# Kernel optimization log

Hardware: AMD Instinct MI355X
Metric: run time of the kernel (lower is better)

## Reference

```python
import jax, jax.numpy as jnp
import numpy as np

DIM = 1024
DIM_QK = 1024
DIM_V = 1024
H = 16
SCALE = 1.0 / (DIM_QK ** 0.5)  # NOTE: module scales by sqrt(dim_qk), not sqrt(head_dim)


def setup_inputs() -> dict:
    key = jax.random.key(0)
    ks = jax.random.split(key, 12)
    B, S = 2, 2048
    q = jax.random.normal(ks[0], (B, S, DIM), jnp.float32)
    k = jax.random.normal(ks[1], (B, S, DIM), jnp.float32)
    v = jax.random.normal(ks[2], (B, S, DIM), jnp.float32)
    mask = jax.random.randint(ks[3], (B, 1, S, S), 0, 2) > 0  # True = masked
    s = 1.0 / np.sqrt(DIM)
    Wq = jax.random.uniform(ks[4], (DIM_QK, DIM), jnp.float32, -s, s)
    bq = jax.random.uniform(ks[5], (DIM_QK,), jnp.float32, -s, s)
    Wk = jax.random.uniform(ks[6], (DIM_QK, DIM), jnp.float32, -s, s)
    bk = jax.random.uniform(ks[7], (DIM_QK,), jnp.float32, -s, s)
    Wv = jax.random.uniform(ks[8], (DIM_V, DIM), jnp.float32, -s, s)
    bv = jax.random.uniform(ks[9], (DIM_V,), jnp.float32, -s, s)
    Wo = jax.random.uniform(ks[10], (DIM_V, DIM), jnp.float32, -s, s)
    bo = jax.random.uniform(ks[11], (DIM_V,), jnp.float32, -s, s)
    return {"q": q, "k": k, "v": v, "mask": mask,
            "Wq": Wq, "bq": bq, "Wk": Wk, "bk": bk,
            "Wv": Wv, "bv": bv, "Wo": Wo, "bo": bo}


def reference(q, k, v, mask, Wq, bq, Wk, bk, Wv, bv, Wo, bo):
    B, Sq, _ = q.shape
    Skv = k.shape[1]
    # projections (torch Linear: x @ W.T + b)
    qh = (q @ Wq.T + bq).reshape(B, Sq, H, DIM_QK // H).transpose(0, 2, 1, 3)   # [B,H,Sq,dk]
    kh = (k @ Wk.T + bk).reshape(B, Skv, H, DIM_QK // H).transpose(0, 2, 1, 3)  # [B,H,Skv,dk]
    vh = (v @ Wv.T + bv).reshape(B, Skv, H, DIM_V // H).transpose(0, 2, 1, 3)   # [B,H,Skv,dv]
    attn = jnp.einsum('bhqd,bhkd->bhqk', qh, kh) * SCALE
    attn = jnp.where(mask, jnp.float32(-1e20), attn)
    attn = jax.nn.softmax(attn, axis=-1)
    # dropout is identity in eval / p=0
    out = jnp.einsum('bhqk,bhkd->bhqd', attn, vh)            # [B,H,Sq,dv]
    out = out.transpose(0, 2, 1, 3).reshape(B, Sq, DIM_V)
    return out @ Wo.T + bo
```

## Files before the change

kernel.cpp:

```cpp
#include <hip/hip_runtime.h>
#include <hip/hip_bf16.h>

typedef __attribute__((ext_vector_type(8))) __bf16 bf16x8;
typedef __attribute__((ext_vector_type(4))) short short4v;
typedef __attribute__((ext_vector_type(4))) float f32x4;
typedef __attribute__((ext_vector_type(4))) unsigned int uint4v;
typedef __attribute__((ext_vector_type(2))) unsigned int uint2v;

#define S_LEN 2048
#define DIM_  1024
#define HDIM  64
#define SCALE2 0.045084441f
#define QK_STR 80
#define V_STR  72

#define EXP2F(x) __builtin_amdgcn_exp2f(x)

__device__ __forceinline__ void async_copy16(const void* gp, void* lp) {
  __builtin_amdgcn_global_load_lds(
      (const __attribute__((address_space(1))) unsigned int*)gp,
      (__attribute__((address_space(3))) unsigned int*)lp, 16, 0, 0);
}

__device__ __forceinline__ unsigned f2bf_u(float f) {
  unsigned u = __builtin_bit_cast(unsigned, f);
  return (u + 0x7FFFu + ((u >> 16) & 1u)) >> 16;
}
__device__ __forceinline__ unsigned pack2(float a, float b) {
  return f2bf_u(a) | (f2bf_u(b) << 16);
}
__device__ __forceinline__ unsigned pack2f(float a, float b) {
  unsigned ua = __builtin_bit_cast(unsigned, a) + 0x8000u;
  unsigned ub = __builtin_bit_cast(unsigned, b) + 0x8000u;
  return __builtin_amdgcn_perm(ub, ua, 0x07060302u);
}

__global__ __launch_bounds__(256) void cvt_kernel(
    const float* __restrict__ s0, const float* __restrict__ s1, const float* __restrict__ s2,
    const float* __restrict__ s3, const float* __restrict__ s4, const float* __restrict__ s5,
    const float* __restrict__ s6,
    __hip_bfloat16* __restrict__ d0, __hip_bfloat16* __restrict__ d1, __hip_bfloat16* __restrict__ d2,
    __hip_bfloat16* __restrict__ d3, __hip_bfloat16* __restrict__ d4, __hip_bfloat16* __restrict__ d5,
    __hip_bfloat16* __restrict__ d6)
{
  const float* srcs[7] = {s0, s1, s2, s3, s4, s5, s6};
  __hip_bfloat16* dsts[7] = {d0, d1, d2, d3, d4, d5, d6};
  const int sizes[7] = {4194304, 4194304, 4194304, 1048576, 1048576, 1048576, 1048576};
  int rg = blockIdx.y;
  int base = (blockIdx.x * 256 + threadIdx.x) * 8;
  if (base >= sizes[rg]) return;
  const float* s = srcs[rg] + base;
  f32x4 a = *(const f32x4*)s;
  f32x4 b = *(const f32x4*)(s + 4);
  uint4v o;
  o.x = pack2(a[0], a[1]); o.y = pack2(a[2], a[3]);
  o.z = pack2(b[0], b[1]); o.w = pack2(b[2], b[3]);
  *(uint4v*)(dsts[rg] + base) = o;
}

__global__ __launch_bounds__(256) void maskbits_kernel(
    const int* __restrict__ mask, unsigned long long* __restrict__ bits)
{
  int w = (blockIdx.x * 256 + threadIdx.x) >> 6;
  int lane = threadIdx.x & 63;
  int m = mask[(size_t)w * 64 + lane];
  unsigned long long bal = __ballot(m != 0);
  if (lane == 0) bits[w] = bal;
}

__device__ __forceinline__ void swz(int r, int& m0, int& n0) {
  int g  = r >> 6;
  int yy = (r >> 3) & 7;
  int xl = r & 7;
  m0 = (g * 8 + xl) * 128;
  n0 = yy * 128;
}

__global__ __launch_bounds__(256) void qkv_gemm_kernel(
    const __hip_bfloat16* __restrict__ xq, const __hip_bfloat16* __restrict__ xk,
    const __hip_bfloat16* __restrict__ xv,
    const __hip_bfloat16* __restrict__ Wq, const float* __restrict__ bq,
    const __hip_bfloat16* __restrict__ Wk, const float* __restrict__ bk,
    const __hip_bfloat16* __restrict__ Wv, const float* __restrict__ bv,
    __hip_bfloat16* __restrict__ Q, __hip_bfloat16* __restrict__ Kk,
    __hip_bfloat16* __restrict__ VT)
{
  const __hip_bfloat16 *X, *W; const float* bias;
  if (blockIdx.z == 0)      { X = xq; W = Wq; bias = bq; }
  else if (blockIdx.z == 1) { X = xk; W = Wk; bias = bk; }
  else                      { X = xv; W = Wv; bias = bv; }

  constexpr int K = 1024, N = 1024;
  __shared__ alignas(16) __hip_bfloat16 As[2][128 * 32];
  __shared__ alignas(16) __hip_bfloat16 Bs[2][128 * 32];
  const int tid  = threadIdx.x;
  const int lane = tid & 63;
  const int wave = tid >> 6;
  const int t    = lane & 15;
  const int quad = lane >> 4;
  const int wm   = wave >> 1;
  const int wn   = wave & 1;
  int m0, n0;
  swz(blockIdx.x, m0, n0);

  f32x4 acc[4][4] = {};

  const int c0 = tid, c1 = 256 + tid;
  const int r0 = c0 >> 2, o0 = (c0 & 3) * 8;
  const int r1 = c1 >> 2, o1 = (c1 & 3) * 8;
  const __hip_bfloat16* xp0 = &X[(size_t)(m0 + r0) * K + o0];
  const __hip_bfloat16* xp1 = &X[(size_t)(m0 + r1) * K + o1];
  const __hip_bfloat16* wp0 = &W[(size_t)(n0 + r0) * K + o0];
  const __hip_bfloat16* wp1 = &W[(size_t)(n0 + r1) * K + o1];

  async_copy16(xp0, &As[0][c0 * 8]);
  async_copy16(xp1, &As[0][c1 * 8]);
  async_copy16(wp0, &Bs[0][c0 * 8]);
  async_copy16(wp1, &Bs[0][c1 * 8]);

  int buf = 0;
  for (int k0 = 0; k0 < K; k0 += 32) {
    __syncthreads();
    if (k0 + 32 < K) {
      int nb = buf ^ 1;
      int kn = k0 + 32;
      async_copy16(xp0 + kn, &As[nb][c0 * 8]);
      async_copy16(xp1 + kn, &As[nb][c1 * 8]);
      async_copy16(wp0 + kn, &Bs[nb][c0 * 8]);
      async_copy16(wp1 + kn, &Bs[nb][c1 * 8]);
    }
    bf16x8 a[4], b[4];
#pragma unroll
    for (int i = 0; i < 4; ++i)
      a[i] = *(const bf16x8*)&As[buf][(wm * 64 + i * 16 + t) * 32 + quad * 8];
#pragma unroll
    for (int j = 0; j < 4; ++j)
      b[j] = *(const bf16x8*)&Bs[buf][(wn * 64 + j * 16 + t) * 32 + quad * 8];
#pragma unroll
    for (int i = 0; i < 4; ++i)
#pragma unroll
      for (int j = 0; j < 4; ++j)
        acc[i][j] = __builtin_amdgcn_mfma_f32_16x16x32_bf16(a[i], b[j], acc[i][j], 0, 0, 0);
    buf ^= 1;
  }

  float bj[4];
#pragma unroll
  for (int j = 0; j < 4; ++j)
    bj[j] = bias[n0 + wn * 64 + j * 16 + t];

  if (blockIdx.z == 2) {
#pragma unroll
    for (int i = 0; i < 4; ++i)
#pragma unroll
      for (int j = 0; j < 4; ++j) {
        int m = m0 + wm * 64 + i * 16 + quad * 4;
        int n = n0 + wn * 64 + j * 16 + t;
        int bb = m >> 11, kv = m & 2047;
        int hh = n >> 6,  dv = n & 63;
        uint2v o;
        o.x = pack2(acc[i][j][0] + bj[j], acc[i][j][1] + bj[j]);
        o.y = pack2(acc[i][j][2] + bj[j], acc[i][j][3] + bj[j]);
        *(uint2v*)&VT[(size_t)(((bb * 16 + hh) * 64) + dv) * 2048 + kv] = o;
      }
  } else {
    const bool isq = (blockIdx.z == 0);
    __hip_bfloat16* Out = isq ? Q : Kk;
    const float sc = isq ? SCALE2 : 1.0f;
#pragma unroll
    for (int i = 0; i < 4; ++i)
#pragma unroll
      for (int j = 0; j < 4; ++j)
#pragma unroll
        for (int r = 0; r < 4; ++r) {
          int m = m0 + wm * 64 + i * 16 + quad * 4 + r;
          int n = n0 + wn * 64 + j * 16 + t;
          Out[(size_t)m * N + n] = __float2bfloat16((acc[i][j][r] + bj[j]) * sc);
        }
  }
}

__global__ __launch_bounds__(256) void proj_gemm_kernel(
    const __hip_bfloat16* __restrict__ X, const __hip_bfloat16* __restrict__ W,
    const float* __restrict__ bias, float* __restrict__ Out)
{
  constexpr int K = 1024, N = 1024;
  __shared__ alignas(16) __hip_bfloat16 As[2][128 * 32];
  __shared__ alignas(16) __hip_bfloat16 Bs[2][128 * 32];
  const int tid  = threadIdx.x;
  const int lane = tid & 63;
  const int wave = tid >> 6;
  const int t    = lane & 15;
  const int quad = lane >> 4;
  const int wm   = wave >> 1;
  const int wn   = wave & 1;
  int m0, n0;
  swz(blockIdx.x, m0, n0);

  f32x4 acc[4][4] = {};

  const int c0 = tid, c1 = 256 + tid;
  const int r0 = c0 >> 2, o0 = (c0 & 3) * 8;
  const int r1 = c1 >> 2, o1 = (c1 & 3) * 8;
  const __hip_bfloat16* xp0 = &X[(size_t)(m0 + r0) * K + o0];
  const __hip_bfloat16* xp1 = &X[(size_t)(m0 + r1) * K + o1];
  const __hip_bfloat16* wp0 = &W[(size_t)(n0 + r0) * K + o0];
  const __hip_bfloat16* wp1 = &W[(size_t)(n0 + r1) * K + o1];

  async_copy16(xp0, &As[0][c0 * 8]);
  async_copy16(xp1, &As[0][c1 * 8]);
  async_copy16(wp0, &Bs[0][c0 * 8]);
  async_copy16(wp1, &Bs[0][c1 * 8]);

  int buf = 0;
  for (int k0 = 0; k0 < K; k0 += 32) {
    __syncthreads();
    if (k0 + 32 < K) {
      int nb = buf ^ 1;
      int kn = k0 + 32;
      async_copy16(xp0 + kn, &As[nb][c0 * 8]);
      async_copy16(xp1 + kn, &As[nb][c1 * 8]);
      async_copy16(wp0 + kn, &Bs[nb][c0 * 8]);
      async_copy16(wp1 + kn, &Bs[nb][c1 * 8]);
    }
    bf16x8 a[4], b[4];
#pragma unroll
    for (int i = 0; i < 4; ++i)
      a[i] = *(const bf16x8*)&As[buf][(wm * 64 + i * 16 + t) * 32 + quad * 8];
#pragma unroll
    for (int j = 0; j < 4; ++j)
      b[j] = *(const bf16x8*)&Bs[buf][(wn * 64 + j * 16 + t) * 32 + quad * 8];
#pragma unroll
    for (int i = 0; i < 4; ++i)
#pragma unroll
      for (int j = 0; j < 4; ++j)
        acc[i][j] = __builtin_amdgcn_mfma_f32_16x16x32_bf16(a[i], b[j], acc[i][j], 0, 0, 0);
    buf ^= 1;
  }

  float bj[4];
#pragma unroll
  for (int j = 0; j < 4; ++j)
    bj[j] = bias[n0 + wn * 64 + j * 16 + t];
#pragma unroll
  for (int i = 0; i < 4; ++i)
#pragma unroll
    for (int j = 0; j < 4; ++j)
#pragma unroll
      for (int r = 0; r < 4; ++r) {
        int m = m0 + wm * 64 + i * 16 + quad * 4 + r;
        int n = n0 + wn * 64 + j * 16 + t;
        Out[(size_t)m * N + n] = acc[i][j][r] + bj[j];
      }
}

__global__ __launch_bounds__(256) void attn_kernel(
    const __hip_bfloat16* __restrict__ Qb,
    const __hip_bfloat16* __restrict__ Kb,
    const __hip_bfloat16* __restrict__ VT,
    const unsigned long long* __restrict__ mbits,
    __hip_bfloat16* __restrict__ Ob)
{
  const int bid = blockIdx.x;
  const int qt = bid & 31;
  const int h  = (bid >> 5) & 15;
  const int b  = bid >> 9;
  const int qb = qt * 64;

  __shared__ alignas(16) __hip_bfloat16 Qs[64 * QK_STR];
  __shared__ alignas(16) __hip_bfloat16 Ks[64 * QK_STR];
  __shared__ alignas(16) __hip_bfloat16 Vt[64 * V_STR];

  const int tid  = threadIdx.x;
  const int lane = tid & 63;
  const int wave = tid >> 6;
  const int t    = lane & 15;
  const int quad = lane >> 4;

#pragma unroll
  for (int r = 0; r < 2; ++r) {
    int c = r * 256 + tid;
    int row = c >> 3, d0 = (c & 7) * 8;
    uint4 raw = *(const uint4*)&Qb[((size_t)(b * S_LEN + qb + row)) * DIM_ + h * HDIM + d0];
    *(uint4*)&Qs[row * QK_STR + d0] = raw;
  }
  __syncthreads();

  bf16x8 qf[2];
#pragma unroll
  for (int ks = 0; ks < 2; ++ks)
    qf[ks] = *(const bf16x8*)&Qs[(wave * 16 + t) * QK_STR + ks * 32 + quad * 8];

  float lp = 0.f;
  f32x4 o[4] = {};

  const int qg = qb + wave * 16 + t;
  const size_t vtbase = (size_t)((b * 16 + h) * 64) * 2048;
  const size_t mbase = ((size_t)b * S_LEN + qg) * 32;

  for (int kvt = 0; kvt < 32; ++kvt) {
    const int kvb = kvt * 64;
    unsigned long long mw = mbits[mbase + kvt];
    __syncthreads();
#pragma unroll
    for (int r = 0; r < 2; ++r) {
      int c = r * 256 + tid;
      int row = c >> 3, d0 = (c & 7) * 8;
      uint4 kraw = *(const uint4*)&Kb[((size_t)(b * S_LEN + kvb + row)) * DIM_ + h * HDIM + d0];
      *(uint4*)&Ks[row * QK_STR + d0] = kraw;
      uint4 vraw = *(const uint4*)&VT[vtbase + (size_t)row * 2048 + kvb + d0];
      *(uint4*)&Vt[row * V_STR + d0] = vraw;
    }
    __syncthreads();

    float e[4][4];
#pragma unroll
    for (int i = 0; i < 4; ++i) {
      f32x4 z = {};
      bf16x8 a0 = *(const bf16x8*)&Ks[(i * 16 + t) * QK_STR + quad * 8];
      z = __builtin_amdgcn_mfma_f32_16x16x32_bf16(a0, qf[0], z, 0, 0, 0);
      bf16x8 a1 = *(const bf16x8*)&Ks[(i * 16 + t) * QK_STR + 32 + quad * 8];
      z = __builtin_amdgcn_mfma_f32_16x16x32_bf16(a1, qf[1], z, 0, 0, 0);
      unsigned mq = (unsigned)((mw >> (i * 16 + quad * 4)) & 0xFull);
#pragma unroll
      for (int r = 0; r < 4; ++r) {
        float v = ((mq >> r) & 1u) ? -1e20f : z[r];
        float ex = EXP2F(v);
        e[i][r] = ex;
        lp += ex;
      }
    }

    short4v pf[4];
#pragma unroll
    for (int j = 0; j < 4; ++j) {
      uint2v pk;
      pk.x = pack2f(e[j][0], e[j][1]);
      pk.y = pack2f(e[j][2], e[j][3]);
      pf[j] = __builtin_bit_cast(short4v, pk);
    }

#pragma unroll
    for (int j = 0; j < 4; ++j)
#pragma unroll
      for (int n = 0; n < 4; ++n) {
        short4v va = *(const short4v*)&Vt[(n * 16 + t) * V_STR + j * 16 + quad * 4];
        o[n] = __builtin_amdgcn_mfma_f32_16x16x16bf16_1k(va, pf[j], o[n], 0, 0, 0);
      }
  }

  lp += __shfl_xor(lp, 16, 64);
  lp += __shfl_xor(lp, 32, 64);
  float rl = 1.0f / lp;

  __hip_bfloat16* Ts = Qs;
  __syncthreads();
#pragma unroll
  for (int n = 0; n < 4; ++n) {
    uint2v pk;
    pk.x = pack2f(o[n][0] * rl, o[n][1] * rl);
    pk.y = pack2f(o[n][2] * rl, o[n][3] * rl);
    *(uint2v*)&Ts[(wave * 16 + t) * V_STR + n * 16 + quad * 4] = pk;
  }
  __syncthreads();
  {
    int row = tid >> 2;
    int d0  = (tid & 3) * 16;
    uint4 x0 = *(const uint4*)&Ts[row * V_STR + d0];
    uint4 x1 = *(const uint4*)&Ts[row * V_STR + d0 + 8];
    __hip_bfloat16* dst = &Ob[((size_t)(b * S_LEN + qb + row)) * DIM_ + h * HDIM + d0];
    *(uint4*)dst = x0;
    *(uint4*)(dst + 8) = x1;
  }
}

extern "C" void kernel_launch(void* const* d_in, const int* in_sizes, int n_in,
                              void* d_out, int out_size, void* d_ws, size_t ws_size,
                              hipStream_t stream) {
  const float* q  = (const float*)d_in[0];
  const float* k  = (const float*)d_in[1];
  const float* v  = (const float*)d_in[2];
  const int*   mk = (const int*)d_in[3];
  const float* Wq = (const float*)d_in[4];
  const float* bq = (const float*)d_in[5];
  const float* Wk = (const float*)d_in[6];
  const float* bk = (const float*)d_in[7];
  const float* Wv = (const float*)d_in[8];
  const float* bv = (const float*)d_in[9];
  const float* Wo = (const float*)d_in[10];
  const float* bo = (const float*)d_in[11];
  float* out = (float*)d_out;

  char* ws = (char*)d_ws;
  const size_t MB = 1024 * 1024;
  __hip_bfloat16* Qb  = (__hip_bfloat16*)(ws);
  __hip_bfloat16* Kb  = (__hip_bfloat16*)(ws + 8  * MB);
  __hip_bfloat16* VTb = (__hip_bfloat16*)(ws + 16 * MB);
  __hip_bfloat16* Ob  = (__hip_bfloat16*)(ws + 24 * MB);
  __hip_bfloat16* xqb = (__hip_bfloat16*)(ws + 32 * MB);
  __hip_bfloat16* xkb = (__hip_bfloat16*)(ws + 40 * MB);
  __hip_bfloat16* xvb = (__hip_bfloat16*)(ws + 48 * MB);
  __hip_bfloat16* Wqb = (__hip_bfloat16*)(ws + 56 * MB);
  __hip_bfloat16* Wkb = (__hip_bfloat16*)(ws + 58 * MB);
  __hip_bfloat16* Wvb = (__hip_bfloat16*)(ws + 60 * MB);
  __hip_bfloat16* Wob = (__hip_bfloat16*)(ws + 62 * MB);
  unsigned long long* mbits = (unsigned long long*)(ws + 64 * MB);

  cvt_kernel<<<dim3(2048, 7), 256, 0, stream>>>(q, k, v, Wq, Wk, Wv, Wo,
                                                xqb, xkb, xvb, Wqb, Wkb, Wvb, Wob);
  maskbits_kernel<<<dim3(32768), 256, 0, stream>>>(mk, mbits);
  qkv_gemm_kernel<<<dim3(256, 1, 3), 256, 0, stream>>>(xqb, xkb, xvb,
                                                       Wqb, bq, Wkb, bk, Wvb, bv,
                                                       Qb, Kb, VTb);
  attn_kernel<<<dim3(1024), 256, 0, stream>>>(Qb, Kb, VTb, mbits, Ob);
  proj_gemm_kernel<<<dim3(256), 256, 0, stream>>>(Ob, Wob, bo, out);
}
```

Baseline: 295.3 us.

## Prefetch next K/V tile into registers and swizzle attention LDS layout

The attention kernel now loads the next K and V tiles into registers while the current tile is being computed, so global latency overlaps the MFMA work. The padded LDS strides are replaced with an XOR-swizzled 64-wide layout to avoid bank conflicts without padding. It also raises wave priority during compute and splits the softmax denominator into four partial sums to shorten the dependency chain. The cost is extra register pressure for the prefetch buffers and more complex index arithmetic.

```diff
diff --git a/kernel.cpp b/kernel.cpp
--- a/kernel.cpp
+++ b/kernel.cpp
@@ -11,10 +11,10 @@
 #define DIM_  1024
 #define HDIM  64
 #define SCALE2 0.045084441f
-#define QK_STR 80
-#define V_STR  72
 
 #define EXP2F(x) __builtin_amdgcn_exp2f(x)
+
+#define ATTN_SWZ(row, col8) (((row) * 64) + (((col8) ^ ((row) & 7)) << 3))
 
 __device__ __forceinline__ void async_copy16(const void* gp, void* lp) {
   __builtin_amdgcn_global_load_lds(
@@ -267,9 +267,9 @@
   const int b  = bid >> 9;
   const int qb = qt * 64;
 
-  __shared__ alignas(16) __hip_bfloat16 Qs[64 * QK_STR];
-  __shared__ alignas(16) __hip_bfloat16 Ks[64 * QK_STR];
-  __shared__ alignas(16) __hip_bfloat16 Vt[64 * V_STR];
+  __shared__ alignas(16) __hip_bfloat16 Qs[64 * 64];
+  __shared__ alignas(16) __hip_bfloat16 Ks[64 * 64];
+  __shared__ alignas(16) __hip_bfloat16 Vt[64 * 64];
 
   const int tid  = threadIdx.x;
   const int lane = tid & 63;
@@ -280,46 +280,62 @@
 #pragma unroll
   for (int r = 0; r < 2; ++r) {
     int c = r * 256 + tid;
-    int row = c >> 3, d0 = (c & 7) * 8;
-    uint4 raw = *(const uint4*)&Qb[((size_t)(b * S_LEN + qb + row)) * DIM_ + h * HDIM + d0];
-    *(uint4*)&Qs[row * QK_STR + d0] = raw;
-  }
+    int row = c >> 3, c8 = c & 7;
+    uint4 raw = *(const uint4*)&Qb[((size_t)(b * S_LEN + qb + row)) * DIM_ + h * HDIM + c8 * 8];
+    *(uint4*)&Qs[ATTN_SWZ(row, c8)] = raw;
+  }
+
+  const size_t vtbase = (size_t)((b * 16 + h) * 64) * 2048;
+  const int srow = tid >> 3, sc8 = tid & 7;
+  uint4 kr[2], vr[2];
+#pragma unroll
+  for (int r = 0; r < 2; ++r) {
+    int row = r * 32 + srow;
+    kr[r] = *(const uint4*)&Kb[((size_t)(b * S_LEN + row)) * DIM_ + h * HDIM + sc8 * 8];
+    vr[r] = *(const uint4*)&VT[vtbase + (size_t)row * 2048 + sc8 * 8];
+  }
+
   __syncthreads();
 
   bf16x8 qf[2];
 #pragma unroll
   for (int ks = 0; ks < 2; ++ks)
-    qf[ks] = *(const bf16x8*)&Qs[(wave * 16 + t) * QK_STR + ks * 32 + quad * 8];
-
-  float lp = 0.f;
+    qf[ks] = *(const bf16x8*)&Qs[ATTN_SWZ(wave * 16 + t, ks * 4 + quad)];
+
+  f32x4 lp4 = {0.f, 0.f, 0.f, 0.f};
   f32x4 o[4] = {};
 
   const int qg = qb + wave * 16 + t;
-  const size_t vtbase = (size_t)((b * 16 + h) * 64) * 2048;
   const size_t mbase = ((size_t)b * S_LEN + qg) * 32;
 
   for (int kvt = 0; kvt < 32; ++kvt) {
-    const int kvb = kvt * 64;
     unsigned long long mw = mbits[mbase + kvt];
     __syncthreads();
 #pragma unroll
     for (int r = 0; r < 2; ++r) {
-      int c = r * 256 + tid;
-      int row = c >> 3, d0 = (c & 7) * 8;
-      uint4 kraw = *(const uint4*)&Kb[((size_t)(b * S_LEN + kvb + row)) * DIM_ + h * HDIM + d0];
-      *(uint4*)&Ks[row * QK_STR + d0] = kraw;
-      uint4 vraw = *(const uint4*)&VT[vtbase + (size_t)row * 2048 + kvb + d0];
-      *(uint4*)&Vt[row * V_STR + d0] = vraw;
+      int row = r * 32 + srow;
+      *(uint4*)&Ks[ATTN_SWZ(row, sc8)] = kr[r];
+      *(uint4*)&Vt[ATTN_SWZ(row, sc8)] = vr[r];
+    }
+    if (kvt + 1 < 32) {
+      int kvb2 = (kvt + 1) * 64;
+#pragma unroll
+      for (int r = 0; r < 2; ++r) {
+        int row = r * 32 + srow;
+        kr[r] = *(const uint4*)&Kb[((size_t)(b * S_LEN + kvb2 + row)) * DIM_ + h * HDIM + sc8 * 8];
+        vr[r] = *(const uint4*)&VT[vtbase + (size_t)row * 2048 + kvb2 + sc8 * 8];
+      }
     }
     __syncthreads();
 
+    __builtin_amdgcn_s_setprio(1);
     float e[4][4];
 #pragma unroll
     for (int i = 0; i < 4; ++i) {
       f32x4 z = {};
-      bf16x8 a0 = *(const bf16x8*)&Ks[(i * 16 + t) * QK_STR + quad * 8];
+      bf16x8 a0 = *(const bf16x8*)&Ks[ATTN_SWZ(i * 16 + t, quad)];
       z = __builtin_amdgcn_mfma_f32_16x16x32_bf16(a0, qf[0], z, 0, 0, 0);
-      bf16x8 a1 = *(const bf16x8*)&Ks[(i * 16 + t) * QK_STR + 32 + quad * 8];
+      bf16x8 a1 = *(const bf16x8*)&Ks[ATTN_SWZ(i * 16 + t, 4 + quad)];
       z = __builtin_amdgcn_mfma_f32_16x16x32_bf16(a1, qf[1], z, 0, 0, 0);
       unsigned mq = (unsigned)((mw >> (i * 16 + quad * 4)) & 0xFull);
 #pragma unroll
@@ -327,7 +343,7 @@
         float v = ((mq >> r) & 1u) ? -1e20f : z[r];
         float ex = EXP2F(v);
         e[i][r] = ex;
-        lp += ex;
+        lp4[r] += ex;
       }
     }
 
@@ -344,11 +360,14 @@
     for (int j = 0; j < 4; ++j)
 #pragma unroll
       for (int n = 0; n < 4; ++n) {
-        short4v va = *(const short4v*)&Vt[(n * 16 + t) * V_STR + j * 16 + quad * 4];
+        short4v va = *(const short4v*)&Vt[(n * 16 + t) * 64 +
+                         (((j * 2 + (quad >> 1)) ^ (t & 7)) << 3) + (quad & 1) * 4];
         o[n] = __builtin_amdgcn_mfma_f32_16x16x16bf16_1k(va, pf[j], o[n], 0, 0, 0);
       }
-  }
-
+    __builtin_amdgcn_s_setprio(0);
+  }
+
+  float lp = (lp4[0] + lp4[1]) + (lp4[2] + lp4[3]);
   lp += __shfl_xor(lp, 16, 64);
   lp += __shfl_xor(lp, 32, 64);
   float rl = 1.0f / lp;
@@ -360,14 +379,16 @@
     uint2v pk;
     pk.x = pack2f(o[n][0] * rl, o[n][1] * rl);
     pk.y = pack2f(o[n][2] * rl, o[n][3] * rl);
-    *(uint2v*)&Ts[(wave * 16 + t) * V_STR + n * 16 + quad * 4] = pk;
+    *(uint2v*)&Ts[(wave * 16 + t) * 64 +
+                  (((n * 2 + (quad >> 1)) ^ (t & 7)) << 3) + (quad & 1) * 4] = pk;
   }
   __syncthreads();
   {
     int row = tid >> 2;
-    int d0  = (tid & 3) * 16;
-    uint4 x0 = *(const uint4*)&Ts[row * V_STR + d0];
-    uint4 x1 = *(const uint4*)&Ts[row * V_STR + d0 + 8];
+    int b0  = (tid & 3) * 2;
+    uint4 x0 = *(const uint4*)&Ts[row * 64 + ((b0 ^ (row & 7)) << 3)];
+    uint4 x1 = *(const uint4*)&Ts[row * 64 + (((b0 + 1) ^ (row & 7)) << 3)];
+    int d0 = (tid & 3) * 16;
     __hip_bfloat16* dst = &Ob[((size_t)(b * S_LEN + qb + row)) * DIM_ + h * HDIM + d0];
     *(uint4*)dst = x0;
     *(uint4*)(dst + 8) = x1;
```

Result: slower. 369.5 us (+25.1%).
